# Kernel tuning notes

Hardware: AMD Instinct MI355X
Metric: run time of the kernel (lower is better)

The kernel has to match this reference:

```python
import jax, jax.numpy as jnp
import numpy as np


def _rbf(X1, X2, log_ls):
    # exp(-||x1-x2||^2 / (2*ls^2)) via the squared-norm expansion
    sq1 = jnp.sum(X1 * X1, axis=-1)[:, None]
    sq2 = jnp.sum(X2 * X2, axis=-1)[None, :]
    d2 = jnp.maximum(sq1 + sq2 - 2.0 * (X1 @ X2.T), 0.0)
    ls2 = jnp.exp(2.0 * log_ls)
    return jnp.exp(-d2 / (2.0 * ls2))


def setup_inputs() -> dict:
    key = jax.random.key(0)
    k1, k2, k3 = jax.random.split(key, 3)
    N_way, K_shot, Q_query, D = 16, 32, 4096, 1024
    Zs = jax.random.normal(k1, (N_way * K_shot, D), dtype=jnp.float32)
    Ys = jax.random.randint(k2, (N_way * K_shot, 1), 0, N_way)
    Zq = jax.random.normal(k3, (N_way * Q_query, D), dtype=jnp.float32)
    log_ls = jnp.asarray(0.0, dtype=jnp.float32)
    log_noise = jnp.asarray(-3.0, dtype=jnp.float32)
    return {"Zs": Zs, "Ys": Ys, "Zq": Zq, "log_ls": log_ls,
            "log_noise": log_noise, "N_way": N_way}


def reference(Zs, Ys, Zq, log_ls, log_noise, N_way):
    Nsamp = Zs.shape[0]  # N_way * K_shot
    Y1hot = jax.nn.one_hot(Ys.reshape(-1), N_way, dtype=Zs.dtype)  # [Nsamp, N_way]
    noise = jnp.exp(2.0 * log_noise)
    Kss = _rbf(Zs, Zs, log_ls) + noise * jnp.eye(Nsamp, dtype=Zs.dtype)
    L = jnp.linalg.cholesky(Kss)
    alpha = jax.scipy.linalg.cho_solve((L, True), Y1hot)  # [Nsamp, N_way]
    Kqs = _rbf(Zq, Zs, log_ls)  # [Q, Nsamp]
    f_q = Kqs @ alpha  # [Q, N_way]
    return jax.nn.softmax(f_q, axis=-1)
```

## Files before the change

kernel.cpp:

```cpp
#include <hip/hip_runtime.h>
#include <math.h>

#define NS 512
#define NQ 65536
#define DD 1024
#define NW 16
#define NWG 36

typedef __attribute__((ext_vector_type(8))) short short8x;
typedef __attribute__((ext_vector_type(4))) float floatx4;

static __device__ __forceinline__ unsigned short bf_trunc(float x) {
  return (unsigned short)(__float_as_uint(x) >> 16);
}
static __device__ __forceinline__ float bf_tof(unsigned short h) {
  return __uint_as_float(((unsigned)h) << 16);
}
static __device__ __forceinline__ unsigned short bf_rne(float x) {
  unsigned u = __float_as_uint(x);
  return (unsigned short)((u + 0x7FFFu + ((u >> 16) & 1u)) >> 16);
}

#define STASH(Hp, Lp, row, k0, v) do {                                      \
    unsigned e_ = (unsigned)((((row) * 32 + (k0)) ^ (((row) & 7) << 3)));   \
    ushort4 h_, l_;                                                         \
    h_.x = bf_trunc((v).x); l_.x = bf_trunc((v).x - bf_tof(h_.x));          \
    h_.y = bf_trunc((v).y); l_.y = bf_trunc((v).y - bf_tof(h_.y));          \
    h_.z = bf_trunc((v).z); l_.z = bf_trunc((v).z - bf_tof(h_.z));          \
    h_.w = bf_trunc((v).w); l_.w = bf_trunc((v).w - bf_tof(h_.w));          \
    *(ushort4*)&Hp[e_] = h_; *(ushort4*)&Lp[e_] = l_;                       \
  } while (0)

__device__ __forceinline__ void gbar(int* cnt, int* gen) {
  __syncthreads();
  if (threadIdx.x == 0) {
    int g = __hip_atomic_load(gen, __ATOMIC_RELAXED, __HIP_MEMORY_SCOPE_AGENT);
    __threadfence();
    int p = __hip_atomic_fetch_add(cnt, 1, __ATOMIC_RELAXED, __HIP_MEMORY_SCOPE_AGENT);
    if (p == NWG - 1) {
      __hip_atomic_store(cnt, 0, __ATOMIC_RELAXED, __HIP_MEMORY_SCOPE_AGENT);
      __hip_atomic_store(gen, g + 1, __ATOMIC_RELEASE, __HIP_MEMORY_SCOPE_AGENT);
    } else {
      while (__hip_atomic_load(gen, __ATOMIC_RELAXED, __HIP_MEMORY_SCOPE_AGENT) == g)
        __builtin_amdgcn_s_sleep(4);
    }
    __threadfence();
  }
  __syncthreads();
}

__device__ __forceinline__ void potrf_tile(const float* T68, float* __restrict__ K, int j) {
  const int tid = threadIdx.x;
  if (tid < 64) {
    const int r = tid;
    float ar[64];
    #pragma unroll
    for (int c4 = 0; c4 < 16; ++c4)
      *(floatx4*)&ar[c4 * 4] = *(const floatx4*)&T68[r * 68 + c4 * 4];
    #pragma unroll
    for (int c = 0; c < 64; ++c) {
      float colv = ar[c];
      float d = __shfl(colv, c);
      float sq = sqrtf(d);
      float inv = 1.f / sq;
      float x = (r > c) ? colv * inv : ((r == c) ? sq : 0.f);
      ar[c] = x;
      #pragma unroll
      for (int k = c + 1; k < 64; ++k) {
        float xk = __shfl(x, k);
        ar[k] = fmaf(-x, xk, ar[k]);
      }
    }
    #pragma unroll
    for (int c = 0; c < 64; ++c) {
      if (c <= r) K[(size_t)(j + r) * NS + j + c] = ar[c];
      if (c < r)  K[(size_t)(j + c) * NS + j + r] = ar[c];
    }
  }
}

__device__ __forceinline__ void solve_lower(const float* P, const float* invd,
                                            const float* __restrict__ Wsrc16,
                                            float* WsT, float* __restrict__ Wg, int j) {
  const int tid = threadIdx.x;
  if (tid < 64) {
    const int n = tid & 15, rq = tid >> 4;
    float w16[16];
    #pragma unroll
    for (int i = 0; i < 16; ++i) w16[i] = Wsrc16[(size_t)(rq + 4 * i) * 16 + n];
    #pragma unroll
    for (int g = 0; g < 16; ++g) {
      floatx4 p[16];
      #pragma unroll
      for (int i = 0; i < 16; ++i) p[i] = *(const floatx4*)&P[(rq + 4 * i) * 68 + 4 * g];
      #pragma unroll
      for (int cj = 0; cj < 4; ++cj) {
        const int c = 4 * g + cj;
        float xc = __shfl(w16[c >> 2], ((c & 3) << 4) + n) * invd[c];
        if (rq == (c & 3)) w16[c >> 2] = xc;
        #pragma unroll
        for (int i = 0; i < 16; ++i) {
          int r = rq + 4 * i;
          if (r > c) w16[i] -= p[i][cj] * xc;
        }
      }
    }
    #pragma unroll
    for (int i = 0; i < 16; ++i) {
      WsT[n * 68 + rq + 4 * i] = w16[i];
      Wg[(size_t)(j + rq + 4 * i) * 16 + n] = w16[i];
    }
  }
}

__device__ __forceinline__ void solve_upper(const float* P, const float* invd,
                                            const float* __restrict__ Wsrc16,
                                            float* __restrict__ Wg, int j) {
  const int tid = threadIdx.x;
  if (tid < 64) {
    const int n = tid & 15, rq = tid >> 4;
    float w16[16];
    #pragma unroll
    for (int i = 0; i < 16; ++i) w16[i] = Wsrc16[(size_t)(rq + 4 * i) * 16 + n];
    #pragma unroll
    for (int g = 15; g >= 0; --g) {
      floatx4 p[16];
      #pragma unroll
      for (int i = 0; i < 16; ++i) p[i] = *(const floatx4*)&P[(rq + 4 * i) * 68 + 4 * g];
      #pragma unroll
      for (int cj = 3; cj >= 0; --cj) {
        const int c = 4 * g + cj;
        float xc = __shfl(w16[c >> 2], ((c & 3) << 4) + n) * invd[c];
        if (rq == (c & 3)) w16[c >> 2] = xc;
        #pragma unroll
        for (int i = 0; i < 16; ++i) {
          int r = rq + 4 * i;
          if (r < c) w16[i] -= p[i][cj] * xc;
        }
      }
    }
    #pragma unroll
    for (int i = 0; i < 16; ++i)
      Wg[(size_t)(j + rq + 4 * i) * 16 + n] = w16[i];
  }
}

__global__ __launch_bounds__(256) void setup_all(const float* __restrict__ Zs,
                                                 const int* __restrict__ Ys,
                                                 const float* __restrict__ log_ls,
                                                 const float* __restrict__ log_noise,
                                                 float* __restrict__ K,
                                                 float* __restrict__ sn,
                                                 float* __restrict__ Wg,
                                                 unsigned short* __restrict__ alpha_t,
                                                 int* cnt, int* gen) {
  __shared__ float pf[13184];
  const int wg = blockIdx.x, tid = threadIdx.x;

  {
    int wave = tid >> 6, lane = tid & 63;
    for (int r = wg * 4 + wave; r < NS; r += NWG * 4) {
      const float* row = Zs + (size_t)r * DD;
      float s = 0.f;
      #pragma unroll
      for (int i = 0; i < 4; ++i) {
        float4 v = *(const float4*)(row + 4 * lane + 256 * i);
        s += v.x * v.x + v.y * v.y + v.z * v.z + v.w * v.w;
      }
      #pragma unroll
      for (int off = 32; off; off >>= 1) s += __shfl_xor(s, off);
      if (lane == 0) sn[r] = s;
    }
    int flat = wg * 256 + tid;
    if (flat < NS * NW) Wg[flat] = (Ys[flat >> 4] == (flat & 15)) ? 1.f : 0.f;
  }
  gbar(cnt, gen);

  {
    int by = 0, accv = 0;
    while (accv + by + 1 <= wg) { accv += by + 1; ++by; }
    int bx = wg - accv;
    const int rb = by * 64, cb = bx * 64;
    float* At = pf;
    float* Bt = pf + 1088;
    float* Tile = pf + 8832;
    const int tx = tid & 15, ty = tid >> 4;
    const int srow = tid & 63, skq = (tid >> 6) << 2;
    float acc[4][4] = {};
    for (int kk = 0; kk < DD; kk += 16) {
      __syncthreads();
      float4 a = *(const float4*)(Zs + (size_t)(rb + srow) * DD + kk + skq);
      float4 b = *(const float4*)(Zs + (size_t)(cb + srow) * DD + kk + skq);
      At[(skq + 0) * 68 + srow] = a.x; At[(skq + 1) * 68 + srow] = a.y;
      At[(skq + 2) * 68 + srow] = a.z; At[(skq + 3) * 68 + srow] = a.w;
      Bt[(skq + 0) * 68 + srow] = b.x; Bt[(skq + 1) * 68 + srow] = b.y;
      Bt[(skq + 2) * 68 + srow] = b.z; Bt[(skq + 3) * 68 + srow] = b.w;
      __syncthreads();
      #pragma unroll
      for (int k = 0; k < 16; ++k) {
        floatx4 av = *(const floatx4*)&At[k * 68 + ty * 4];
        floatx4 bv = *(const floatx4*)&Bt[k * 68 + tx * 4];
        #pragma unroll
        for (int i = 0; i < 4; ++i)
          #pragma unroll
          for (int jj = 0; jj < 4; ++jj)
            acc[i][jj] = fmaf(av[i], bv[jj], acc[i][jj]);
      }
    }
    float inv2 = 0.5f * expf(-2.f * log_ls[0]);
    float noise = expf(2.f * log_noise[0]);
    #pragma unroll
    for (int i = 0; i < 4; ++i)
      #pragma unroll
      for (int jj = 0; jj < 4; ++jj) {
        int r = rb + ty * 4 + i, c = cb + tx * 4 + jj;
        float d2 = fmaxf(sn[r] + sn[c] - 2.f * acc[i][jj], 0.f);
        float v = expf(-d2 * inv2);
        if (r == c) v += noise;
        K[(size_t)r * NS + c] = v;
        if (wg == 0) Tile[(ty * 4 + i) * 68 + tx * 4 + jj] = v;
      }
    if (wg == 0) {
      __syncthreads();
      potrf_tile(Tile, K, 0);
    }
  }
  gbar(cnt, gen);

  for (int jb = 0; jb < 7; ++jb) {
    const int j = jb << 6;
    {
      float* Ld = pf;
      float* invd = pf + 4416;
      #pragma unroll
      for (int it = 0; it < 4; ++it) {
        int flat = tid + 256 * it;
        int r = flat >> 4, c4 = (flat & 15) * 4;
        *(floatx4*)&Ld[r * 68 + c4] = *(const floatx4*)&K[(size_t)(j + r) * NS + j + c4];
      }
      __syncthreads();
      if (tid < 64) invd[tid] = 1.f / Ld[tid * 68 + tid];
      __syncthreads();
      const int r0 = j + 64 + wg + NWG * tid;
      if (r0 < NS) {
        float xr[64];
        #pragma unroll
        for (int c4 = 0; c4 < 16; ++c4)
          *(floatx4*)&xr[c4 * 4] = *(const floatx4*)&K[(size_t)r0 * NS + j + c4 * 4];
        #pragma unroll
        for (int g = 0; g < 16; ++g) {
          float v0 = xr[4 * g], v1 = xr[4 * g + 1], v2 = xr[4 * g + 2], v3 = xr[4 * g + 3];
          for (int kb = 0; kb < g; ++kb) {
            floatx4 x4 = *(const floatx4*)&xr[4 * kb];
            floatx4 l0 = *(const floatx4*)&Ld[(4 * g + 0) * 68 + 4 * kb];
            floatx4 l1 = *(const floatx4*)&Ld[(4 * g + 1) * 68 + 4 * kb];
            floatx4 l2 = *(const floatx4*)&Ld[(4 * g + 2) * 68 + 4 * kb];
            floatx4 l3 = *(const floatx4*)&Ld[(4 * g + 3) * 68 + 4 * kb];
            v0 -= x4.x * l0.x + x4.y * l0.y + x4.z * l0.z + x4.w * l0.w;
            v1 -= x4.x * l1.x + x4.y * l1.y + x4.z * l1.z + x4.w * l1.w;
            v2 -= x4.x * l2.x + x4.y * l2.y + x4.z * l2.z + x4.w * l2.w;
            v3 -= x4.x * l3.x + x4.y * l3.y + x4.z * l3.z + x4.w * l3.w;
          }
          const int c0 = 4 * g;
          float x0 = v0 * invd[c0];
          v1 -= x0 * Ld[(c0 + 1) * 68 + c0];
          float x1 = v1 * invd[c0 + 1];
          v2 -= x0 * Ld[(c0 + 2) * 68 + c0] + x1 * Ld[(c0 + 2) * 68 + c0 + 1];
          float x2 = v2 * invd[c0 + 2];
          v3 -= x0 * Ld[(c0 + 3) * 68 + c0] + x1 * Ld[(c0 + 3) * 68 + c0 + 1] + x2 * Ld[(c0 + 3) * 68 + c0 + 2];
          float x3 = v3 * invd[c0 + 3];
          xr[c0] = x0; xr[c0 + 1] = x1; xr[c0 + 2] = x2; xr[c0 + 3] = x3;
        }
        #pragma unroll
        for (int c4 = 0; c4 < 16; ++c4)
          *(floatx4*)(K + (size_t)r0 * NS + j + c4 * 4) = *(const floatx4*)&xr[c4 * 4];
        #pragma unroll
        for (int c = 0; c < 64; ++c)
          K[(size_t)(j + c) * NS + r0] = xr[c];
      }
    }
    gbar(cnt, gen);

    {
      const int T = 7 - jb;
      const int nt = T * (T + 1) / 2;
      if (wg < nt) {
        int ti = 0, a2 = 0;
        while (a2 + ti + 1 <= wg) { a2 += ti + 1; ++ti; }
        int tj = wg - a2;
        const int rbt = j + 64 + ti * 64, cbt = j + 64 + tj * 64;
        float* A = pf;
        float* B = pf + 4416;
        float* Tile = pf + 8832;
        for (int i = tid; i < 4096; i += 256) {
          int r = i >> 6, k = i & 63;
          A[r * 69 + k] = K[(size_t)(rbt + r) * NS + j + k];
          B[r * 69 + k] = K[(size_t)(cbt + r) * NS + j + k];
        }
        __syncthreads();
        const int tx = tid & 15, ty = tid >> 4;
        float acc[4][4] = {};
        for (int k = 0; k < 64; ++k) {
          float aa[4], bb[4];
          #pragma unroll
          for (int i = 0; i < 4; ++i) aa[i] = A[(ty * 4 + i) * 69 + k];
          #pragma unroll
          for (int i = 0; i < 4; ++i) bb[i] = B[(tx * 4 + i) * 69 + k];
          #pragma unroll
          for (int i = 0; i < 4; ++i)
            #pragma unroll
            for (int jj = 0; jj < 4; ++jj)
              acc[i][jj] = fmaf(aa[i], bb[jj], acc[i][jj]);
        }
        #pragma unroll
        for (int i = 0; i < 4; ++i)
          #pragma unroll
          for (int jj = 0; jj < 4; ++jj) {
            float* cp = &K[(size_t)(rbt + ty * 4 + i) * NS + cbt + tx * 4 + jj];
            float nv = *cp - acc[i][jj];
            *cp = nv;
            if (wg == 0) Tile[(ty * 4 + i) * 68 + tx * 4 + jj] = nv;
          }
        if (wg == 0) {
          __syncthreads();
          potrf_tile(Tile, K, j + 64);
        }
      } else if (wg == 35) {
        float* P = pf;
        float* invd = pf + 4416;
        float* WsT = pf + 5504;
        #pragma unroll
        for (int it = 0; it < 4; ++it) {
          int flat = tid + 256 * it;
          int r = flat >> 4, c4 = (flat & 15) * 4;
          *(floatx4*)&P[r * 68 + c4] = *(const floatx4*)&K[(size_t)(j + r) * NS + j + c4];
        }
        __syncthreads();
        if (tid < 64) invd[tid] = 1.f / P[tid * 68 + tid];
        solve_lower(P, invd, Wg + (size_t)j * 16, WsT, Wg, j);
        __syncthreads();
        const int nrows = NS - j - 64;
        for (int flat = tid; flat < nrows * 16; flat += 256) {
          int row = j + 64 + (flat >> 4), nn = flat & 15;
          float s = Wg[(size_t)row * 16 + nn];
          const float* lrow = &K[(size_t)row * NS + j];
          #pragma unroll
          for (int g = 0; g < 16; ++g) {
            floatx4 lv = *(const floatx4*)&lrow[4 * g];
            floatx4 wv = *(const floatx4*)&WsT[nn * 68 + 4 * g];
            s -= lv.x * wv.x + lv.y * wv.y + lv.z * wv.z + lv.w * wv.w;
          }
          Wg[(size_t)row * 16 + nn] = s;
        }
      }
    }
    gbar(cnt, gen);
  }

  {
    const int j = 448;
    if (wg == 35) {
      float* P = pf;
      float* invd = pf + 4416;
      float* WsT = pf + 5504;
      #pragma unroll
      for (int it = 0; it < 4; ++it) {
        int flat = tid + 256 * it;
        int r = flat >> 4, c4 = (flat & 15) * 4;
        *(floatx4*)&P[r * 68 + c4] = *(const floatx4*)&K[(size_t)(j + r) * NS + j + c4];
      }
      __syncthreads();
      if (tid < 64) invd[tid] = 1.f / P[tid * 68 + tid];
      solve_lower(P, invd, Wg + (size_t)j * 16, WsT, Wg, j);
      solve_upper(P, invd, Wg + (size_t)j * 16, Wg, j);
    }
  }
  gbar(cnt, gen);

  for (int jb = 7; jb >= 1; --jb) {
    const int j = jb << 6;
    {
      float* Wst = pf;
      for (int e = tid; e < 1024; e += 256) {
        int c = e >> 4, n = e & 15;
        Wst[n * 68 + c] = Wg[(size_t)(j + c) * 16 + n];
      }
      __syncthreads();
      const int row = wg + NWG * (tid >> 4);
      const int nn = tid & 15;
      if (row < j) {
        float s = Wg[(size_t)row * 16 + nn];
        const float* lrow = &K[(size_t)row * NS + j];
        #pragma unroll
        for (int g = 0; g < 16; ++g) {
          floatx4 lv = *(const floatx4*)&lrow[4 * g];
          floatx4 wv = *(const floatx4*)&Wst[nn * 68 + 4 * g];
          s -= lv.x * wv.x + lv.y * wv.y + lv.z * wv.z + lv.w * wv.w;
        }
        Wg[(size_t)row * 16 + nn] = s;
      }
    }
    gbar(cnt, gen);
    {
      const int j2 = (jb - 1) << 6;
      if (wg == 35) {
        float* P = pf;
        float* invd = pf + 4416;
        #pragma unroll
        for (int it = 0; it < 4; ++it) {
          int flat = tid + 256 * it;
          int r = flat >> 4, c4 = (flat & 15) * 4;
          *(floatx4*)&P[r * 68 + c4] = *(const floatx4*)&K[(size_t)(j2 + r) * NS + j2 + c4];
        }
        __syncthreads();
        if (tid < 64) invd[tid] = 1.f / P[tid * 68 + tid];
        solve_upper(P, invd, Wg + (size_t)j2 * 16, Wg, j2);
      }
    }
    gbar(cnt, gen);
  }

  {
    int flat = wg * 256 + tid;
    if (flat < NS * NW) {
      int r = flat >> 4, nn = flat & 15;
      alpha_t[(size_t)nn * NS + r] = bf_rne(Wg[(size_t)r * 16 + nn]);
    }
  }
}

__global__ __launch_bounds__(512) void fused_v2(const float* __restrict__ Zq,
                                                const float* __restrict__ Zs,
                                                const float* __restrict__ sn,
                                                const unsigned short* __restrict__ alpha_t,
                                                const float* __restrict__ log_ls,
                                                float* __restrict__ out) {
  __shared__ __align__(16) unsigned short LB[32768];
  __shared__ float qnl[128];
  __shared__ float snl[256];
  unsigned short* AhB = LB;
  unsigned short* AlB = LB + 4096;
  unsigned short* BhB = LB + 8192;
  unsigned short* BlB = LB + 16384;
  unsigned short* KqB = LB;

  const int tid = threadIdx.x;
  const int lane = tid & 63;
  const int w = tid >> 6;
  const int wm = w >> 2, wn = w & 3;
  const int l15 = lane & 15, l4 = lane >> 4;
  const int rb = blockIdx.x * 128;
  const float inv2 = 0.5f * __expf(-2.f * log_ls[0]);
  const unsigned swz = (unsigned)((l15 & 7) << 3);

  if (tid < 128) qnl[tid] = 0.f;
  __syncthreads();

  const int qrow0 = tid >> 3;
  const int qk0 = (tid & 7) * 4;
  const int qrow1 = 64 + qrow0;

  floatx4 facc = {0.f, 0.f, 0.f, 0.f};

  for (int cc = 0; cc < NS; cc += 256) {
    if (tid < 256) snl[tid] = sn[cc + tid];
    floatx4 acc[4][4];
    #pragma unroll
    for (int a = 0; a < 4; ++a)
      #pragma unroll
      for (int b = 0; b < 4; ++b) acc[a][b] = (floatx4){0.f, 0.f, 0.f, 0.f};

    float4 pq0 = *(const float4*)(Zq + (size_t)(rb + qrow0) * DD + qk0);
    float4 pq1 = *(const float4*)(Zq + (size_t)(rb + qrow1) * DD + qk0);
    float4 ps[4];
    #pragma unroll
    for (int u = 0; u < 4; ++u) {
      int idx = tid + (u << 9);
      ps[u] = *(const float4*)(Zs + (size_t)(cc + (idx >> 3)) * DD + ((idx & 7) * 4));
    }

    for (int kt = 0; kt < 32; ++kt) {
      STASH(AhB, AlB, qrow0, qk0, pq0);
      STASH(AhB, AlB, qrow1, qk0, pq1);
      #pragma unroll
      for (int u = 0; u < 4; ++u) {
        int idx = tid + (u << 9);
        int srow = idx >> 3, sk0 = (idx & 7) * 4;
        STASH(BhB, BlB, srow, sk0, ps[u]);
      }
      if (cc == 0) {
        float s0 = pq0.x * pq0.x + pq0.y * pq0.y + pq0.z * pq0.z + pq0.w * pq0.w;
        float s1 = pq1.x * pq1.x + pq1.y * pq1.y + pq1.z * pq1.z + pq1.w * pq1.w;
        #pragma unroll
        for (int d = 1; d < 8; d <<= 1) { s0 += __shfl_xor(s0, d); s1 += __shfl_xor(s1, d); }
        if ((tid & 7) == 0) { qnl[qrow0] += s0; qnl[qrow1] += s1; }
      }
      __syncthreads();
      if (kt < 31) {
        int kk2 = (kt + 1) << 5;
        pq0 = *(const float4*)(Zq + (size_t)(rb + qrow0) * DD + kk2 + qk0);
        pq1 = *(const float4*)(Zq + (size_t)(rb + qrow1) * DD + kk2 + qk0);
        #pragma unroll
        for (int u = 0; u < 4; ++u) {
          int idx = tid + (u << 9);
          ps[u] = *(const float4*)(Zs + (size_t)(cc + (idx >> 3)) * DD + kk2 + ((idx & 7) * 4));
        }
      }
      short8x ah[4], al[4], bh[4], bl[4];
      #pragma unroll
      for (int mi = 0; mi < 4; ++mi) {
        unsigned e = (unsigned)((wm * 64 + mi * 16 + l15) * 32 + 8 * l4) ^ swz;
        ah[mi] = *(const short8x*)&AhB[e];
        al[mi] = *(const short8x*)&AlB[e];
      }
      #pragma unroll
      for (int ni = 0; ni < 4; ++ni) {
        unsigned e = (unsigned)((wn * 64 + ni * 16 + l15) * 32 + 8 * l4) ^ swz;
        bh[ni] = *(const short8x*)&BhB[e];
        bl[ni] = *(const short8x*)&BlB[e];
      }
      #pragma unroll
      for (int mi = 0; mi < 4; ++mi)
        #pragma unroll
        for (int ni = 0; ni < 4; ++ni) {
          acc[mi][ni] = __builtin_amdgcn_mfma_f32_16x16x32_bf16(ah[mi], bh[ni], acc[mi][ni], 0, 0, 0);
          acc[mi][ni] = __builtin_amdgcn_mfma_f32_16x16x32_bf16(ah[mi], bl[ni], acc[mi][ni], 0, 0, 0);
          acc[mi][ni] = __builtin_amdgcn_mfma_f32_16x16x32_bf16(al[mi], bh[ni], acc[mi][ni], 0, 0, 0);
        }
      __syncthreads();
    }

    short8x bfr[8];
    #pragma unroll
    for (int s = 0; s < 8; ++s)
      bfr[s] = *(const short8x*)(alpha_t + ((size_t)l15 * NS + cc + 32 * s + 8 * l4));

    #pragma unroll
    for (int mi = 0; mi < 4; ++mi)
      #pragma unroll
      for (int rr = 0; rr < 4; ++rr) {
        int row_l = wm * 64 + mi * 16 + l4 * 4 + rr;
        float qv = qnl[row_l];
        unsigned sw = (unsigned)((row_l & 7) << 3);
        #pragma unroll
        for (int ni = 0; ni < 4; ++ni) {
          int col = wn * 64 + ni * 16 + l15;
          float d2 = fmaxf(qv + snl[col] - 2.f * acc[mi][ni][rr], 0.f);
          float kq = __expf(-d2 * inv2);
          KqB[(unsigned)(row_l * 256 + col) ^ sw] = bf_rne(kq);
        }
      }
    __syncthreads();
    #pragma unroll
    for (int s = 0; s < 8; ++s) {
      unsigned e = (unsigned)((w * 16 + l15) * 256 + 32 * s + 8 * l4) ^ swz;
      short8x ak = *(const short8x*)&KqB[e];
      facc = __builtin_amdgcn_mfma_f32_16x16x32_bf16(ak, bfr[s], facc, 0, 0, 0);
    }
    __syncthreads();
  }

  #pragma unroll
  for (int r = 0; r < 4; ++r) {
    float v = facc[r];
    float m = v;
    #pragma unroll
    for (int d = 1; d < 16; d <<= 1) m = fmaxf(m, __shfl_xor(m, d));
    float e = __expf(v - m);
    float s = e;
    #pragma unroll
    for (int d = 1; d < 16; d <<= 1) s += __shfl_xor(s, d);
    out[(size_t)(rb + w * 16 + l4 * 4 + r) * NW + l15] = e / s;
  }
}

extern "C" void kernel_launch(void* const* d_in, const int* in_sizes, int n_in,
                              void* d_out, int out_size, void* d_ws, size_t ws_size,
                              hipStream_t stream) {
  (void)in_sizes; (void)n_in; (void)out_size; (void)ws_size;
  const float* Zs = (const float*)d_in[0];
  const int*   Ys = (const int*)d_in[1];
  const float* Zq = (const float*)d_in[2];
  const float* log_ls = (const float*)d_in[3];
  const float* log_noise = (const float*)d_in[4];
  float* out = (float*)d_out;

  float* ws = (float*)d_ws;
  float* K  = ws;
  float* sn = ws + (size_t)NS * NS;
  unsigned short* alpha_t = (unsigned short*)(sn + NS);
  float* Wg = sn + NS + 4096;
  int* flags = (int*)(Wg + (size_t)NS * NW);

  hipMemsetAsync(flags, 0, 2 * sizeof(int), stream);
  setup_all<<<NWG, 256, 0, stream>>>(Zs, Ys, log_ls, log_noise, K, sn, Wg, alpha_t,
                                     flags, flags + 1);
  fused_v2<<<NQ / 128, 512, 0, stream>>>(Zq, Zs, sn, alpha_t, log_ls, out);
}
```

Measured before the change: 1.708 ms.

## Fuse panel TRSM into trailing update and cut grid barriers in Cholesky setup

The setup kernel now folds the squared-norm pass into the Gram tile stage, so one grid barrier goes away. Each trailing-update workgroup recomputes the triangular solve for its own panel rows instead of waiting on a separate TRSM phase and barrier. The forward solve is pipelined one block behind on workgroup 35, and the backward solve runs entirely on workgroup 0 using the stored transposed and row panel copies (LT, Lrow). This removes about half of the grid-wide barriers in the serial setup. In exchange it adds redundant TRSM work, extra workspace, and a long single-workgroup tail for the backward solve.

```diff
diff --git a/kernel.cpp b/kernel.cpp
--- a/kernel.cpp
+++ b/kernel.cpp
@@ -79,6 +79,38 @@
   }
 }
 
+__device__ __forceinline__ void trsm_row(const float* __restrict__ Krow,
+                                         const float* Ld, const float* invd,
+                                         float* xr) {
+  #pragma unroll
+  for (int c4 = 0; c4 < 16; ++c4)
+    *(floatx4*)&xr[c4 * 4] = *(const floatx4*)(Krow + c4 * 4);
+  #pragma unroll
+  for (int g = 0; g < 16; ++g) {
+    float v0 = xr[4 * g + 0], v1 = xr[4 * g + 1], v2 = xr[4 * g + 2], v3 = xr[4 * g + 3];
+    for (int kb = 0; kb < g; ++kb) {
+      floatx4 x4 = *(const floatx4*)&xr[4 * kb];
+      floatx4 l0 = *(const floatx4*)&Ld[(4 * g + 0) * 68 + 4 * kb];
+      floatx4 l1 = *(const floatx4*)&Ld[(4 * g + 1) * 68 + 4 * kb];
+      floatx4 l2 = *(const floatx4*)&Ld[(4 * g + 2) * 68 + 4 * kb];
+      floatx4 l3 = *(const floatx4*)&Ld[(4 * g + 3) * 68 + 4 * kb];
+      v0 -= x4.x * l0.x + x4.y * l0.y + x4.z * l0.z + x4.w * l0.w;
+      v1 -= x4.x * l1.x + x4.y * l1.y + x4.z * l1.z + x4.w * l1.w;
+      v2 -= x4.x * l2.x + x4.y * l2.y + x4.z * l2.z + x4.w * l2.w;
+      v3 -= x4.x * l3.x + x4.y * l3.y + x4.z * l3.z + x4.w * l3.w;
+    }
+    const int c0 = 4 * g;
+    float x0 = v0 * invd[c0];
+    v1 -= x0 * Ld[(c0 + 1) * 68 + c0];
+    float x1 = v1 * invd[c0 + 1];
+    v2 -= x0 * Ld[(c0 + 2) * 68 + c0] + x1 * Ld[(c0 + 2) * 68 + c0 + 1];
+    float x2 = v2 * invd[c0 + 2];
+    v3 -= x0 * Ld[(c0 + 3) * 68 + c0] + x1 * Ld[(c0 + 3) * 68 + c0 + 1] + x2 * Ld[(c0 + 3) * 68 + c0 + 2];
+    float x3 = v3 * invd[c0 + 3];
+    xr[c0] = x0; xr[c0 + 1] = x1; xr[c0 + 2] = x2; xr[c0 + 3] = x3;
+  }
+}
+
 __device__ __forceinline__ void solve_lower(const float* P, const float* invd,
                                             const float* __restrict__ Wsrc16,
                                             float* WsT, float* __restrict__ Wg, int j) {
@@ -145,45 +177,49 @@
   }
 }
 
-__global__ __launch_bounds__(256) void setup_all(const float* __restrict__ Zs,
-                                                 const int* __restrict__ Ys,
-                                                 const float* __restrict__ log_ls,
-                                                 const float* __restrict__ log_noise,
-                                                 float* __restrict__ K,
-                                                 float* __restrict__ sn,
-                                                 float* __restrict__ Wg,
-                                                 unsigned short* __restrict__ alpha_t,
-                                                 int* cnt, int* gen) {
-  __shared__ float pf[13184];
+__global__ __launch_bounds__(256) void setup_v3(const float* __restrict__ Zs,
+                                                const int* __restrict__ Ys,
+                                                const float* __restrict__ log_ls,
+                                                const float* __restrict__ log_noise,
+                                                float* __restrict__ K,
+                                                float* __restrict__ sn,
+                                                float* __restrict__ Wg,
+                                                float* __restrict__ LT,
+                                                float* __restrict__ Lrow,
+                                                unsigned short* __restrict__ alpha_t,
+                                                int* cnt, int* gen) {
+  __shared__ float pf[13056];
+  __shared__ float invd[64];
   const int wg = blockIdx.x, tid = threadIdx.x;
 
+  int by = 0, accv = 0;
+  while (accv + by + 1 <= wg) { accv += by + 1; ++by; }
+  const int bx = wg - accv;
+
   {
-    int wave = tid >> 6, lane = tid & 63;
-    for (int r = wg * 4 + wave; r < NS; r += NWG * 4) {
-      const float* row = Zs + (size_t)r * DD;
-      float s = 0.f;
-      #pragma unroll
-      for (int i = 0; i < 4; ++i) {
-        float4 v = *(const float4*)(row + 4 * lane + 256 * i);
-        s += v.x * v.x + v.y * v.y + v.z * v.z + v.w * v.w;
-      }
-      #pragma unroll
-      for (int off = 32; off; off >>= 1) s += __shfl_xor(s, off);
-      if (lane == 0) sn[r] = s;
-    }
-    int flat = wg * 256 + tid;
-    if (flat < NS * NW) Wg[flat] = (Ys[flat >> 4] == (flat & 15)) ? 1.f : 0.f;
-  }
-  gbar(cnt, gen);
-
-  {
-    int by = 0, accv = 0;
-    while (accv + by + 1 <= wg) { accv += by + 1; ++by; }
-    int bx = wg - accv;
     const int rb = by * 64, cb = bx * 64;
-    float* At = pf;
-    float* Bt = pf + 1088;
-    float* Tile = pf + 8832;
+    float* snl = pf;
+    float* At = pf + 128;
+    float* Bt = pf + 1216;
+    float* Tile = pf + 2304;
+    if (tid < 128) {
+      int row = (tid < 64) ? rb + tid : cb + (tid - 64);
+      const float4* rp = (const float4*)(Zs + (size_t)row * DD);
+      float s0 = 0.f, s1 = 0.f, s2 = 0.f, s3 = 0.f;
+      for (int i = 0; i < 256; i += 4) {
+        float4 a = rp[i], b2 = rp[i + 1], c2 = rp[i + 2], d2 = rp[i + 3];
+        s0 += a.x * a.x + a.y * a.y + a.z * a.z + a.w * a.w;
+        s1 += b2.x * b2.x + b2.y * b2.y + b2.z * b2.z + b2.w * b2.w;
+        s2 += c2.x * c2.x + c2.y * c2.y + c2.z * c2.z + c2.w * c2.w;
+        s3 += d2.x * d2.x + d2.y * d2.y + d2.z * d2.z + d2.w * d2.w;
+      }
+      snl[tid] = (s0 + s1) + (s2 + s3);
+      if (by == bx && tid < 64) sn[rb + tid] = snl[tid];
+    }
+    {
+      int flat = wg * 256 + tid;
+      if (flat < NS * NW) Wg[flat] = (Ys[flat >> 4] == (flat & 15)) ? 1.f : 0.f;
+    }
     const int tx = tid & 15, ty = tid >> 4;
     const int srow = tid & 63, skq = (tid >> 6) << 2;
     float acc[4][4] = {};
@@ -213,12 +249,13 @@
     for (int i = 0; i < 4; ++i)
       #pragma unroll
       for (int jj = 0; jj < 4; ++jj) {
-        int r = rb + ty * 4 + i, c = cb + tx * 4 + jj;
-        float d2 = fmaxf(sn[r] + sn[c] - 2.f * acc[i][jj], 0.f);
+        int rl = ty * 4 + i, cl = tx * 4 + jj;
+        int r = rb + rl, c = cb + cl;
+        float d2 = fmaxf(snl[rl] + snl[64 + cl] - 2.f * acc[i][jj], 0.f);
         float v = expf(-d2 * inv2);
         if (r == c) v += noise;
         K[(size_t)r * NS + c] = v;
-        if (wg == 0) Tile[(ty * 4 + i) * 68 + tx * 4 + jj] = v;
+        if (wg == 0) Tile[rl * 68 + cl] = v;
       }
     if (wg == 0) {
       __syncthreads();
@@ -229,9 +266,16 @@
 
   for (int jb = 0; jb < 7; ++jb) {
     const int j = jb << 6;
-    {
+    const int T = 7 - jb;
+    const int nt = T * (T + 1) / 2;
+    if (wg < nt) {
+      int ti = 0, a2 = 0;
+      while (a2 + ti + 1 <= wg) { a2 += ti + 1; ++ti; }
+      const int tj = wg - a2;
+      const int rbt = j + 64 + ti * 64, cbt = j + 64 + tj * 64;
       float* Ld = pf;
-      float* invd = pf + 4416;
+      float* A  = pf + 4352;
+      float* B  = (ti == tj) ? A : pf + 8704;
       #pragma unroll
       for (int it = 0; it < 4; ++it) {
         int flat = tid + 256 * it;
@@ -241,77 +285,47 @@
       __syncthreads();
       if (tid < 64) invd[tid] = 1.f / Ld[tid * 68 + tid];
       __syncthreads();
-      const int r0 = j + 64 + wg + NWG * tid;
-      if (r0 < NS) {
+      if (tid < 64) {
         float xr[64];
+        const int row = rbt + tid;
+        trsm_row(&K[(size_t)row * NS + j], Ld, invd, xr);
         #pragma unroll
         for (int c4 = 0; c4 < 16; ++c4)
-          *(floatx4*)&xr[c4 * 4] = *(const floatx4*)&K[(size_t)r0 * NS + j + c4 * 4];
-        #pragma unroll
-        for (int g = 0; g < 16; ++g) {
-          float v0 = xr[4 * g], v1 = xr[4 * g + 1], v2 = xr[4 * g + 2], v3 = xr[4 * g + 3];
-          for (int kb = 0; kb < g; ++kb) {
-            floatx4 x4 = *(const floatx4*)&xr[4 * kb];
-            floatx4 l0 = *(const floatx4*)&Ld[(4 * g + 0) * 68 + 4 * kb];
-            floatx4 l1 = *(const floatx4*)&Ld[(4 * g + 1) * 68 + 4 * kb];
-            floatx4 l2 = *(const floatx4*)&Ld[(4 * g + 2) * 68 + 4 * kb];
-            floatx4 l3 = *(const floatx4*)&Ld[(4 * g + 3) * 68 + 4 * kb];
-            v0 -= x4.x * l0.x + x4.y * l0.y + x4.z * l0.z + x4.w * l0.w;
-            v1 -= x4.x * l1.x + x4.y * l1.y + x4.z * l1.z + x4.w * l1.w;
-            v2 -= x4.x * l2.x + x4.y * l2.y + x4.z * l2.z + x4.w * l2.w;
-            v3 -= x4.x * l3.x + x4.y * l3.y + x4.z * l3.z + x4.w * l3.w;
-          }
-          const int c0 = 4 * g;
-          float x0 = v0 * invd[c0];
-          v1 -= x0 * Ld[(c0 + 1) * 68 + c0];
-          float x1 = v1 * invd[c0 + 1];
-          v2 -= x0 * Ld[(c0 + 2) * 68 + c0] + x1 * Ld[(c0 + 2) * 68 + c0 + 1];
-          float x2 = v2 * invd[c0 + 2];
-          v3 -= x0 * Ld[(c0 + 3) * 68 + c0] + x1 * Ld[(c0 + 3) * 68 + c0 + 1] + x2 * Ld[(c0 + 3) * 68 + c0 + 2];
-          float x3 = v3 * invd[c0 + 3];
-          xr[c0] = x0; xr[c0 + 1] = x1; xr[c0 + 2] = x2; xr[c0 + 3] = x3;
-        }
+          *(floatx4*)&A[tid * 68 + c4 * 4] = *(const floatx4*)&xr[c4 * 4];
+        if (tj == 0) {
+          float* lr = Lrow + ((size_t)jb * NS + row) * 64;
+          #pragma unroll
+          for (int c4 = 0; c4 < 16; ++c4)
+            *(floatx4*)(lr + c4 * 4) = *(const floatx4*)&xr[c4 * 4];
+          #pragma unroll
+          for (int c = 0; c < 64; ++c)
+            LT[(size_t)(j + c) * NS + row] = xr[c];
+        }
+      } else if (tid < 128 && ti != tj) {
+        float xr[64];
+        const int row = cbt + (tid - 64);
+        trsm_row(&K[(size_t)row * NS + j], Ld, invd, xr);
         #pragma unroll
         for (int c4 = 0; c4 < 16; ++c4)
-          *(floatx4*)(K + (size_t)r0 * NS + j + c4 * 4) = *(const floatx4*)&xr[c4 * 4];
-        #pragma unroll
-        for (int c = 0; c < 64; ++c)
-          K[(size_t)(j + c) * NS + r0] = xr[c];
-      }
-    }
-    gbar(cnt, gen);
-
-    {
-      const int T = 7 - jb;
-      const int nt = T * (T + 1) / 2;
-      if (wg < nt) {
-        int ti = 0, a2 = 0;
-        while (a2 + ti + 1 <= wg) { a2 += ti + 1; ++ti; }
-        int tj = wg - a2;
-        const int rbt = j + 64 + ti * 64, cbt = j + 64 + tj * 64;
-        float* A = pf;
-        float* B = pf + 4416;
-        float* Tile = pf + 8832;
-        for (int i = tid; i < 4096; i += 256) {
-          int r = i >> 6, k = i & 63;
-          A[r * 69 + k] = K[(size_t)(rbt + r) * NS + j + k];
-          B[r * 69 + k] = K[(size_t)(cbt + r) * NS + j + k];
-        }
-        __syncthreads();
+          *(floatx4*)&B[(tid - 64) * 68 + c4 * 4] = *(const floatx4*)&xr[c4 * 4];
+      }
+      __syncthreads();
+      {
         const int tx = tid & 15, ty = tid >> 4;
         float acc[4][4] = {};
         for (int k = 0; k < 64; ++k) {
           float aa[4], bb[4];
           #pragma unroll
-          for (int i = 0; i < 4; ++i) aa[i] = A[(ty * 4 + i) * 69 + k];
-          #pragma unroll
-          for (int i = 0; i < 4; ++i) bb[i] = B[(tx * 4 + i) * 69 + k];
+          for (int i = 0; i < 4; ++i) aa[i] = A[(ty * 4 + i) * 68 + k];
+          #pragma unroll
+          for (int i = 0; i < 4; ++i) bb[i] = B[(tx * 4 + i) * 68 + k];
           #pragma unroll
           for (int i = 0; i < 4; ++i)
             #pragma unroll
             for (int jj = 0; jj < 4; ++jj)
               acc[i][jj] = fmaf(aa[i], bb[jj], acc[i][jj]);
         }
+        __syncthreads();
         #pragma unroll
         for (int i = 0; i < 4; ++i)
           #pragma unroll
@@ -319,113 +333,113 @@
             float* cp = &K[(size_t)(rbt + ty * 4 + i) * NS + cbt + tx * 4 + jj];
             float nv = *cp - acc[i][jj];
             *cp = nv;
-            if (wg == 0) Tile[(ty * 4 + i) * 68 + tx * 4 + jj] = nv;
+            if (wg == 0) Ld[(ty * 4 + i) * 68 + tx * 4 + jj] = nv;
           }
-        if (wg == 0) {
-          __syncthreads();
-          potrf_tile(Tile, K, j + 64);
-        }
-      } else if (wg == 35) {
-        float* P = pf;
-        float* invd = pf + 4416;
-        float* WsT = pf + 5504;
-        #pragma unroll
-        for (int it = 0; it < 4; ++it) {
-          int flat = tid + 256 * it;
-          int r = flat >> 4, c4 = (flat & 15) * 4;
-          *(floatx4*)&P[r * 68 + c4] = *(const floatx4*)&K[(size_t)(j + r) * NS + j + c4];
-        }
+      }
+      if (wg == 0) {
         __syncthreads();
-        if (tid < 64) invd[tid] = 1.f / P[tid * 68 + tid];
-        solve_lower(P, invd, Wg + (size_t)j * 16, WsT, Wg, j);
-        __syncthreads();
-        const int nrows = NS - j - 64;
-        for (int flat = tid; flat < nrows * 16; flat += 256) {
-          int row = j + 64 + (flat >> 4), nn = flat & 15;
+        potrf_tile(Ld, K, j + 64);
+      }
+    } else if (wg == 35 && jb >= 1) {
+      const int b = jb - 1, j2 = b << 6;
+      float* P = pf;
+      float* WsT = pf + 4352;
+      #pragma unroll
+      for (int it = 0; it < 4; ++it) {
+        int flat = tid + 256 * it;
+        int r = flat >> 4, c4 = (flat & 15) * 4;
+        *(floatx4*)&P[r * 68 + c4] = *(const floatx4*)&K[(size_t)(j2 + r) * NS + j2 + c4];
+      }
+      __syncthreads();
+      if (tid < 64) invd[tid] = 1.f / P[tid * 68 + tid];
+      solve_lower(P, invd, Wg + (size_t)j2 * 16, WsT, Wg, j2);
+      __syncthreads();
+      const int nrows = NS - j2 - 64;
+      for (int flat = tid; flat < nrows * 16; flat += 256) {
+        int row = j2 + 64 + (flat >> 4), nn = flat & 15;
+        float s = Wg[(size_t)row * 16 + nn];
+        const float* lr = Lrow + ((size_t)b * NS + row) * 64;
+        #pragma unroll
+        for (int g = 0; g < 16; ++g) {
+          floatx4 lv = *(const floatx4*)(lr + 4 * g);
+          floatx4 wv = *(const floatx4*)&WsT[nn * 68 + 4 * g];
+          s -= lv.x * wv.x + lv.y * wv.y + lv.z * wv.z + lv.w * wv.w;
+        }
+        Wg[(size_t)row * 16 + nn] = s;
+      }
+    }
+    gbar(cnt, gen);
+  }
+
+  if (wg != 0) return;
+  {
+    float* P = pf;
+    float* WsT = pf + 4352;
+    for (int b = 6; b <= 7; ++b) {
+      const int j2 = b << 6;
+      __syncthreads();
+      #pragma unroll
+      for (int it = 0; it < 4; ++it) {
+        int flat = tid + 256 * it;
+        int r = flat >> 4, c4 = (flat & 15) * 4;
+        *(floatx4*)&P[r * 68 + c4] = *(const floatx4*)&K[(size_t)(j2 + r) * NS + j2 + c4];
+      }
+      __syncthreads();
+      if (tid < 64) invd[tid] = 1.f / P[tid * 68 + tid];
+      solve_lower(P, invd, Wg + (size_t)j2 * 16, WsT, Wg, j2);
+      __syncthreads();
+      if (b == 6) {
+        for (int flat = tid; flat < 64 * 16; flat += 256) {
+          int row = 448 + (flat >> 4), nn = flat & 15;
           float s = Wg[(size_t)row * 16 + nn];
-          const float* lrow = &K[(size_t)row * NS + j];
+          const float* lr = Lrow + ((size_t)6 * NS + row) * 64;
           #pragma unroll
           for (int g = 0; g < 16; ++g) {
-            floatx4 lv = *(const floatx4*)&lrow[4 * g];
+            floatx4 lv = *(const floatx4*)(lr + 4 * g);
             floatx4 wv = *(const floatx4*)&WsT[nn * 68 + 4 * g];
             s -= lv.x * wv.x + lv.y * wv.y + lv.z * wv.z + lv.w * wv.w;
           }
           Wg[(size_t)row * 16 + nn] = s;
         }
-      }
-    }
-    gbar(cnt, gen);
-  }
-
-  {
-    const int j = 448;
-    if (wg == 35) {
-      float* P = pf;
-      float* invd = pf + 4416;
-      float* WsT = pf + 5504;
+        __syncthreads();
+      }
+    }
+    for (int jb2 = 7; jb2 >= 0; --jb2) {
+      const int j2 = jb2 << 6;
+      __syncthreads();
       #pragma unroll
       for (int it = 0; it < 4; ++it) {
         int flat = tid + 256 * it;
         int r = flat >> 4, c4 = (flat & 15) * 4;
-        *(floatx4*)&P[r * 68 + c4] = *(const floatx4*)&K[(size_t)(j + r) * NS + j + c4];
+        *(floatx4*)&P[r * 68 + c4] = *(const floatx4*)&K[(size_t)(j2 + r) * NS + j2 + c4];
       }
       __syncthreads();
       if (tid < 64) invd[tid] = 1.f / P[tid * 68 + tid];
-      solve_lower(P, invd, Wg + (size_t)j * 16, WsT, Wg, j);
-      solve_upper(P, invd, Wg + (size_t)j * 16, Wg, j);
-    }
-  }
-  gbar(cnt, gen);
-
-  for (int jb = 7; jb >= 1; --jb) {
-    const int j = jb << 6;
-    {
-      float* Wst = pf;
-      for (int e = tid; e < 1024; e += 256) {
-        int c = e >> 4, n = e & 15;
-        Wst[n * 68 + c] = Wg[(size_t)(j + c) * 16 + n];
-      }
-      __syncthreads();
-      const int row = wg + NWG * (tid >> 4);
-      const int nn = tid & 15;
-      if (row < j) {
-        float s = Wg[(size_t)row * 16 + nn];
-        const float* lrow = &K[(size_t)row * NS + j];
-        #pragma unroll
-        for (int g = 0; g < 16; ++g) {
-          floatx4 lv = *(const floatx4*)&lrow[4 * g];
-          floatx4 wv = *(const floatx4*)&Wst[nn * 68 + 4 * g];
-          s -= lv.x * wv.x + lv.y * wv.y + lv.z * wv.z + lv.w * wv.w;
-        }
-        Wg[(size_t)row * 16 + nn] = s;
-      }
-    }
-    gbar(cnt, gen);
-    {
-      const int j2 = (jb - 1) << 6;
-      if (wg == 35) {
-        float* P = pf;
-        float* invd = pf + 4416;
-        #pragma unroll
-        for (int it = 0; it < 4; ++it) {
-          int flat = tid + 256 * it;
-          int r = flat >> 4, c4 = (flat & 15) * 4;
-          *(floatx4*)&P[r * 68 + c4] = *(const floatx4*)&K[(size_t)(j2 + r) * NS + j2 + c4];
+      solve_upper(P, invd, Wg + (size_t)j2 * 16, Wg, j2);
+      __syncthreads();
+      if (jb2 > 0) {
+        for (int e = tid; e < 1024; e += 256) {
+          int c = e >> 4, n = e & 15;
+          WsT[n * 68 + c] = Wg[(size_t)(j2 + c) * 16 + n];
         }
         __syncthreads();
-        if (tid < 64) invd[tid] = 1.f / P[tid * 68 + tid];
-        solve_upper(P, invd, Wg + (size_t)j2 * 16, Wg, j2);
-      }
-    }
-    gbar(cnt, gen);
-  }
-
-  {
-    int flat = wg * 256 + tid;
-    if (flat < NS * NW) {
-      int r = flat >> 4, nn = flat & 15;
-      alpha_t[(size_t)nn * NS + r] = bf_rne(Wg[(size_t)r * 16 + nn]);
-    }
+        for (int flat = tid; flat < j2 * 16; flat += 256) {
+          int r = flat >> 4, nn = flat & 15;
+          float s = Wg[(size_t)r * 16 + nn];
+          const float* lr = LT + (size_t)r * NS + j2;
+          #pragma unroll
+          for (int g = 0; g < 16; ++g) {
+            floatx4 lv = *(const floatx4*)(lr + 4 * g);
+            floatx4 wv = *(const floatx4*)&WsT[nn * 68 + 4 * g];
+            s -= lv.x * wv.x + lv.y * wv.y + lv.z * wv.z + lv.w * wv.w;
+          }
+          Wg[(size_t)r * 16 + nn] = s;
+        }
+        __syncthreads();
+      }
+    }
+    for (int i = tid; i < NS * NW; i += 256)
+      alpha_t[(size_t)(i & 15) * NS + (i >> 4)] = bf_rne(Wg[i]);
   }
 }
 
@@ -587,13 +601,15 @@
 
   float* ws = (float*)d_ws;
   float* K  = ws;
-  float* sn = ws + (size_t)NS * NS;
+  float* sn = K + (size_t)NS * NS;
   unsigned short* alpha_t = (unsigned short*)(sn + NS);
-  float* Wg = sn + NS + 4096;
-  int* flags = (int*)(Wg + (size_t)NS * NW);
+  float* Wg   = sn + NS + 4096;
+  float* LT   = Wg + (size_t)NS * NW;
+  float* Lrow = LT + (size_t)NS * NS;
+  int* flags = (int*)(Lrow + (size_t)8 * NS * 64);
 
   hipMemsetAsync(flags, 0, 2 * sizeof(int), stream);
-  setup_all<<<NWG, 256, 0, stream>>>(Zs, Ys, log_ls, log_noise, K, sn, Wg, alpha_t,
-                                     flags, flags + 1);
+  setup_v3<<<NWG, 256, 0, stream>>>(Zs, Ys, log_ls, log_noise, K, sn, Wg, LT, Lrow,
+                                    alpha_t, flags, flags + 1);
   fused_v2<<<NQ / 128, 512, 0, stream>>>(Zq, Zs, sn, alpha_t, log_ls, out);
 }
```

Result: faster. 1.663 ms (-2.6%).
